# Kernel optimization log

Measured on AMD Instinct MI355X. Metric: run time of the kernel, lower is better.

The kernel has to match this reference:

```python
import jax, jax.numpy as jnp
import numpy as np
import math

# Equal-size graphs make SAGPooling's top-k static; removed edges are kept with a validity mask.
B, N0, D, H, HID, POS, DEG = 64, 400, 128, 4, 64, 16, 16
C = D // H                     # per-head dim = 32
EG = N0 * DEG                  # edges per graph
E = B * EG                     # 409600 edges total
RATIO = 0.8
K1 = math.ceil(RATIO * N0)     # 320
K2 = math.ceil(RATIO * K1)     # 256
K3 = math.ceil(RATIO * K2)     # 205
KS = (K1, K2, K3)
EPS = 1e-5

def _lin(x, W, b):
    return x @ W + b

def _ln(x, g, b):
    mu = x.mean(-1, keepdims=True)
    var = ((x - mu) ** 2).mean(-1, keepdims=True)
    return (x - mu) * jax.lax.rsqrt(var + EPS) * g + b

def _bn(x, g, b):  # BatchNorm1d, training mode (biased batch variance)
    mu = x.mean(0)
    var = ((x - mu) ** 2).mean(0)
    return (x - mu) * jax.lax.rsqrt(var + EPS) * g + b

def _transformer_conv(x, src, dst, mask, Wq, bq, Wk, bk, Wv, bv, Ws, bs, N):
    # PyG TransformerConv (concat=True, root_weight=True): scatter-softmax attention over edges
    q = _lin(x, Wq, bq).reshape(N, H, C)
    k = _lin(x, Wk, bk).reshape(N, H, C)
    v = _lin(x, Wv, bv).reshape(N, H, C)
    logits = jnp.einsum('ehc,ehc->eh', q[dst], k[src]) / jnp.sqrt(jnp.float32(C))
    logits = jnp.where(mask[:, None], logits, -1e9)
    m = jnp.maximum(jax.ops.segment_max(logits, dst, num_segments=N), -1e9)
    w = jnp.exp(logits - m[dst]) * mask[:, None]
    denom = jax.ops.segment_sum(w, dst, num_segments=N)
    alpha = w / jnp.where(denom[dst] > 0, denom[dst], 1.0)  # [E,H]
    msg = jax.ops.segment_sum(v[src] * alpha[:, :, None], dst, num_segments=N)
    return msg.reshape(N, D) + _lin(x, Ws, bs)

def _gt_block(x, src, dst, mask, Wq, bq, Wk, bk, Wv, bv, Ws, bs,
              Wlo, blo, g1, be1, W1, b1, W2, b2, g2, be2, N):
    out1 = _lin(_transformer_conv(x, src, dst, mask, Wq, bq, Wk, bk, Wv, bv, Ws, bs, N), Wlo, blo)
    out2 = _ln(out1 + x, g1, be1)
    out3 = _lin(jax.nn.relu(_lin(out2, W1, b1)), W2, b2)
    return _ln(out3 + out2, g2, be2)

def _sag_pool(x, src, dst, mask, Wrel, brel, Wroot, n, k):
    # SAGPooling: GraphConv(aggr='add') scorer, tanh nonlinearity, per-graph top-k, filter_adj via mask
    Nn = B * n
    agg = jax.ops.segment_sum(x[src] * mask[:, None], dst, num_segments=Nn)
    s = jnp.tanh((agg @ Wrel + brel + x @ Wroot)[:, 0])
    tv, ti = jax.lax.top_k(s.reshape(B, n), k)  # [B,k]
    perm = (ti + jnp.arange(B, dtype=ti.dtype)[:, None] * n).reshape(-1)
    x_new = x[perm] * tv.reshape(-1, 1)
    kept = jnp.zeros(Nn, bool).at[perm].set(True)
    new_id = jnp.zeros(Nn, jnp.int32).at[perm].set(jnp.arange(B * k, dtype=jnp.int32))
    nm = mask & kept[src] & kept[dst]
    return x_new, jnp.where(nm, new_id[src], 0), jnp.where(nm, new_id[dst], 0), nm

def _forward(x, lap_pos_enc, W_pos, b_pos,
             gt_Wq, gt_bq, gt_Wk, gt_bk, gt_Wv, gt_bv, gt_Wskip, gt_bskip,
             gt_Wlo, gt_blo, gt_ln1g, gt_ln1b, gt_W1, gt_b1, gt_W2, gt_b2, gt_ln2g, gt_ln2b,
             pool_Wrel, pool_brel, pool_Wroot,
             hW1, hb1, hW2, hb2, hW3, hb3, bn1g, bn1b, bn2g, bn2b,
             edge_src, edge_dst):
    x = x + _lin(lap_pos_enc, W_pos, b_pos)
    src, dst = edge_src, edge_dst
    mask = jnp.ones(src.shape, bool)
    n = N0
    feats = []
    for i in range(3):
        x = _gt_block(x, src, dst, mask,
                      gt_Wq[i], gt_bq[i], gt_Wk[i], gt_bk[i], gt_Wv[i], gt_bv[i],
                      gt_Wskip[i], gt_bskip[i], gt_Wlo[i], gt_blo[i],
                      gt_ln1g[i], gt_ln1b[i], gt_W1[i], gt_b1[i], gt_W2[i], gt_b2[i],
                      gt_ln2g[i], gt_ln2b[i], B * n)
        x, src, dst, mask = _sag_pool(x, src, dst, mask, pool_Wrel[i], pool_brel[i], pool_Wroot[i], n, KS[i])
        n = KS[i]
        xg = x.reshape(B, n, D)
        feats.append(jnp.concatenate([xg.max(1), xg.mean(1)], axis=1))  # [B, 2D] = gmp | gap
    xf = feats[0] + feats[1] + feats[2]
    h = jax.nn.relu(_bn(_lin(xf, hW1, hb1), bn1g, bn1b))
    h = jax.nn.relu(_bn(_lin(h, hW2, hb2), bn2g, bn2b))
    return _lin(h, hW3, hb3)[:, 0]  # [B]

def setup_inputs():
    key = jax.random.key(0)
    ks = jax.random.split(key, 16)
    rn = lambda k, shape, fan: jax.random.normal(k, shape, jnp.float32) / np.float32(np.sqrt(fan))
    inp = {}
    inp['x'] = jax.random.normal(ks[0], (B * N0, D), jnp.float32)
    inp['lap_pos_enc'] = jax.random.normal(ks[1], (B * N0, POS), jnp.float32)
    offs = (jnp.arange(B, dtype=jnp.int32) * N0)[:, None]
    inp['edge_src'] = (jax.random.randint(ks[2], (B, EG), 0, N0, jnp.int32) + offs).reshape(-1)
    inp['edge_dst'] = (jax.random.randint(ks[3], (B, EG), 0, N0, jnp.int32) + offs).reshape(-1)
    inp['W_pos'] = rn(ks[4], (POS, D), POS); inp['b_pos'] = jnp.zeros(D)
    pk = jax.random.split(ks[5], 12)
    inp['gt_Wq'] = rn(pk[0], (3, D, D), D); inp['gt_bq'] = jnp.zeros((3, D))
    inp['gt_Wk'] = rn(pk[1], (3, D, D), D); inp['gt_bk'] = jnp.zeros((3, D))
    inp['gt_Wv'] = rn(pk[2], (3, D, D), D); inp['gt_bv'] = jnp.zeros((3, D))
    inp['gt_Wskip'] = rn(pk[3], (3, D, D), D); inp['gt_bskip'] = jnp.zeros((3, D))
    inp['gt_Wlo'] = rn(pk[4], (3, D, D), D); inp['gt_blo'] = jnp.zeros((3, D))
    inp['gt_ln1g'] = jnp.ones((3, D)); inp['gt_ln1b'] = jnp.zeros((3, D))
    inp['gt_W1'] = rn(pk[5], (3, D, HID), D); inp['gt_b1'] = jnp.zeros((3, HID))
    inp['gt_W2'] = rn(pk[6], (3, HID, D), HID); inp['gt_b2'] = jnp.zeros((3, D))
    inp['gt_ln2g'] = jnp.ones((3, D)); inp['gt_ln2b'] = jnp.zeros((3, D))
    inp['pool_Wrel'] = rn(pk[7], (3, D, 1), D); inp['pool_brel'] = jnp.zeros((3, 1))
    inp['pool_Wroot'] = rn(pk[8], (3, D, 1), D)
    inp['hW1'] = rn(pk[9], (2 * D, D), 2 * D); inp['hb1'] = jnp.zeros(D)
    inp['hW2'] = rn(pk[10], (D, D // 2), D); inp['hb2'] = jnp.zeros(D // 2)
    inp['hW3'] = rn(pk[11], (D // 2, 1), D // 2); inp['hb3'] = jnp.zeros(1)
    inp['bn1g'] = jnp.ones(D); inp['bn1b'] = jnp.zeros(D)
    inp['bn2g'] = jnp.ones(D // 2); inp['bn2b'] = jnp.zeros(D // 2)
    return inp

def reference(x, lap_pos_enc, edge_src, edge_dst, W_pos, b_pos,
              gt_Wq, gt_bq, gt_Wk, gt_bk, gt_Wv, gt_bv, gt_Wskip, gt_bskip,
              gt_Wlo, gt_blo, gt_ln1g, gt_ln1b, gt_W1, gt_b1, gt_W2, gt_b2, gt_ln2g, gt_ln2b,
              pool_Wrel, pool_brel, pool_Wroot,
              hW1, hb1, hW2, hb2, hW3, hb3, bn1g, bn1b, bn2g, bn2b):
    return _forward(x, lap_pos_enc, W_pos, b_pos,
                    gt_Wq, gt_bq, gt_Wk, gt_bk, gt_Wv, gt_bv, gt_Wskip, gt_bskip,
                    gt_Wlo, gt_blo, gt_ln1g, gt_ln1b, gt_W1, gt_b1, gt_W2, gt_b2, gt_ln2g, gt_ln2b,
                    pool_Wrel, pool_brel, pool_Wroot,
                    hW1, hb1, hW2, hb2, hW3, hb3, bn1g, bn1b, bn2g, bn2b,
                    edge_src, edge_dst)
```

## Files before the change

### kernel.cpp

```cpp
#include <hip/hip_runtime.h>
#include <math.h>

#define BB   64
#define NPG0 400
#define DD   128
#define HH   4
#define CC   32
#define HIDD 64
#define POSD 16
#define EE   409600
#define EG   6400

__global__ void k_pos(const float* __restrict__ x, const float* __restrict__ lap,
                      const float* __restrict__ Wp, const float* __restrict__ bp,
                      float* __restrict__ out, int N){
  __shared__ float W[POSD*DD];
  __shared__ float bsh[DD];
  for(int i=threadIdx.x;i<POSD*DD;i+=blockDim.x) W[i]=Wp[i];
  for(int i=threadIdx.x;i<DD;i+=blockDim.x) bsh[i]=bp[i];
  __syncthreads();
  int total=N*DD;
  for(int idx=blockIdx.x*blockDim.x+threadIdx.x; idx<total; idx+=gridDim.x*blockDim.x){
    int n=idx>>7, d=idx&127;
    const float* lr=lap+(size_t)n*POSD;
    float acc=bsh[d]+x[idx];
    #pragma unroll
    for(int p=0;p<POSD;p++) acc=fmaf(lr[p],W[p*DD+d],acc);
    out[idx]=acc;
  }
}


template<int DIN,int DOUT,int EPI>
__global__ __launch_bounds__(512) void k_gemm_sw(
    const float* __restrict__ X, const float* __restrict__ Wg,
    const float* __restrict__ bias, const float* __restrict__ resid,
    const float* __restrict__ gam, const float* __restrict__ bet,
    float* __restrict__ Y){
  constexpr int CPW=DOUT/8;
  constexpr int NCG=CPW/4;
  constexpr int XPAD=DIN+4;
  __shared__ float Xl[64*XPAD];
  __shared__ float redA[8*64];
  __shared__ float redB[8*64];
  int tid=threadIdx.x;
  { const float4* xs=(const float4*)(X+(size_t)blockIdx.x*64*DIN);
    for(int i=tid;i<64*DIN/4;i+=512){
      int r=i/(DIN/4), kq=i%(DIN/4);
      *(float4*)&Xl[r*XPAD+kq*4]=xs[i];
    } }
  __syncthreads();
  int lane=tid&63;
  int wv=__builtin_amdgcn_readfirstlane(tid>>6);
  int cbase=wv*CPW;
  float acc[CPW];
  #pragma unroll
  for(int c=0;c<CPW;c++) acc[c]=0.f;
  const float* xr=&Xl[lane*XPAD];
  #pragma unroll 2
  for(int kt=0;kt<DIN/4;kt++){
    float4 xv=*(const float4*)&xr[4*kt];
    float xk[4]={xv.x,xv.y,xv.z,xv.w};
    #pragma unroll
    for(int kk=0;kk<4;kk++){
      const float4* wrow=(const float4*)(Wg+(size_t)(4*kt+kk)*DOUT+cbase);
      #pragma unroll
      for(int cg=0;cg<NCG;cg++){
        float4 w4=wrow[cg];
        acc[cg*4+0]=fmaf(xk[kk],w4.x,acc[cg*4+0]);
        acc[cg*4+1]=fmaf(xk[kk],w4.y,acc[cg*4+1]);
        acc[cg*4+2]=fmaf(xk[kk],w4.z,acc[cg*4+2]);
        acc[cg*4+3]=fmaf(xk[kk],w4.w,acc[cg*4+3]);
      }
    }
  }
  int row=blockIdx.x*64+lane;
  const float4* bb4=(const float4*)(bias+cbase);
  #pragma unroll
  for(int cg=0;cg<NCG;cg++){
    float4 b4=bb4[cg];
    acc[cg*4+0]+=b4.x; acc[cg*4+1]+=b4.y; acc[cg*4+2]+=b4.z; acc[cg*4+3]+=b4.w;
  }
  if(EPI==1){
    #pragma unroll
    for(int c=0;c<CPW;c++) acc[c]=fmaxf(acc[c],0.f);
  }
  if(EPI==2){
    #pragma unroll
    for(int cg=0;cg<NCG;cg++){
      float4 rv=*(const float4*)&resid[(size_t)row*DOUT+cbase+cg*4];
      acc[cg*4+0]+=rv.x; acc[cg*4+1]+=rv.y; acc[cg*4+2]+=rv.z; acc[cg*4+3]+=rv.w;
    }
    float ps=0.f,pq=0.f;
    #pragma unroll
    for(int c=0;c<CPW;c++){ ps+=acc[c]; pq+=acc[c]*acc[c]; }
    redA[wv*64+lane]=ps; redB[wv*64+lane]=pq;
    __syncthreads();
    float s=0.f,q=0.f;
    #pragma unroll
    for(int w=0;w<8;w++){ s+=redA[w*64+lane]; q+=redB[w*64+lane]; }
    float mu=s*(1.f/DOUT);
    float var=q*(1.f/DOUT)-mu*mu;
    float inv=1.0f/sqrtf(var+1e-5f);
    const float4* g4p=(const float4*)(gam+cbase);
    const float4* e4p=(const float4*)(bet+cbase);
    #pragma unroll
    for(int cg=0;cg<NCG;cg++){
      float4 g4=g4p[cg], e4=e4p[cg];
      acc[cg*4+0]=(acc[cg*4+0]-mu)*inv*g4.x+e4.x;
      acc[cg*4+1]=(acc[cg*4+1]-mu)*inv*g4.y+e4.y;
      acc[cg*4+2]=(acc[cg*4+2]-mu)*inv*g4.z+e4.z;
      acc[cg*4+3]=(acc[cg*4+3]-mu)*inv*g4.w+e4.w;
    }
  }
  #pragma unroll
  for(int cg=0;cg<NCG;cg++){
    float4 v; v.x=acc[cg*4+0]; v.y=acc[cg*4+1]; v.z=acc[cg*4+2]; v.w=acc[cg*4+3];
    *(float4*)&Y[(size_t)row*DOUT+cbase+cg*4]=v;
  }
}

__global__ __launch_bounds__(512) void k_gemm4_sw(
    const float* __restrict__ X,
    const float* __restrict__ W0,const float* __restrict__ W1,
    const float* __restrict__ W2,const float* __restrict__ W3,
    const float* __restrict__ b0,const float* __restrict__ b1,
    const float* __restrict__ b2,const float* __restrict__ b3,
    float* __restrict__ Y0,float* __restrict__ Y1,
    float* __restrict__ Y2,float* __restrict__ Y3){
  constexpr int XPAD=DD+4;
  __shared__ float Xl[64*XPAD];
  int tid=threadIdx.x;
  { const float4* xs=(const float4*)(X+(size_t)blockIdx.x*64*DD);
    for(int i=tid;i<64*32;i+=512){
      int r=i>>5, kq=i&31;
      *(float4*)&Xl[r*XPAD+kq*4]=xs[i];
    } }
  __syncthreads();
  int lane=tid&63;
  int wv=__builtin_amdgcn_readfirstlane(tid>>6);
  int cbase=wv*16;
  int row=blockIdx.x*64+lane;
  const float* xr=&Xl[lane*XPAD];
  auto one=[&](const float* __restrict__ Wg,const float* __restrict__ bias,float* __restrict__ Y){
    float acc[16];
    #pragma unroll
    for(int c=0;c<16;c++) acc[c]=0.f;
    #pragma unroll 2
    for(int kt=0;kt<32;kt++){
      float4 xv=*(const float4*)&xr[4*kt];
      float xk[4]={xv.x,xv.y,xv.z,xv.w};
      #pragma unroll
      for(int kk=0;kk<4;kk++){
        const float4* wrow=(const float4*)(Wg+(size_t)(4*kt+kk)*DD+cbase);
        #pragma unroll
        for(int cg=0;cg<4;cg++){
          float4 w4=wrow[cg];
          acc[cg*4+0]=fmaf(xk[kk],w4.x,acc[cg*4+0]);
          acc[cg*4+1]=fmaf(xk[kk],w4.y,acc[cg*4+1]);
          acc[cg*4+2]=fmaf(xk[kk],w4.z,acc[cg*4+2]);
          acc[cg*4+3]=fmaf(xk[kk],w4.w,acc[cg*4+3]);
        }
      }
    }
    const float4* bb4=(const float4*)(bias+cbase);
    #pragma unroll
    for(int cg=0;cg<4;cg++){
      float4 b4=bb4[cg];
      float4 v;
      v.x=acc[cg*4+0]+b4.x; v.y=acc[cg*4+1]+b4.y;
      v.z=acc[cg*4+2]+b4.z; v.w=acc[cg*4+3]+b4.w;
      *(float4*)&Y[(size_t)row*DD+cbase+cg*4]=v;
    }
  };
  one(W0,b0,Y0);
  one(W1,b1,Y1);
  one(W2,b2,Y2);
  one(W3,b3,Y3);
}

__global__ __launch_bounds__(512) void k_csr(const int* __restrict__ src,const int* __restrict__ dst,
   const int* __restrict__ msk,const int* __restrict__ kept,const int* __restrict__ nid,int n,
   int* __restrict__ rowstart,int* __restrict__ rowcnt,int* __restrict__ esrc,
   int* __restrict__ nsrc,int* __restrict__ ndst,int* __restrict__ nmsk){
  __shared__ int cnt[512];
  __shared__ int woff[512];
  int b=blockIdx.x, t=threadIdx.x;
  cnt[t]=0;
  __syncthreads();
  int ebase=b*EG, nbase=b*n;
  for(int j=t;j<EG;j+=512){
    int e=ebase+j;
    int s,d,m;
    if(kept){
      int s0=src[e], d0=dst[e];
      m=(msk?msk[e]:1) && kept[s0] && kept[d0];
      s=m?nid[s0]:0; d=m?nid[d0]:0;
      nsrc[e]=s; ndst[e]=d; nmsk[e]=m;
    } else { s=src[e]; d=dst[e]; m=1; }
    if(m) atomicAdd(&cnt[d-nbase],1);
  }
  __syncthreads();
  int v=cnt[t];
  woff[t]=v;
  __syncthreads();
  for(int off=1;off<512;off<<=1){
    int a=(t>=off)?woff[t-off]:0;
    __syncthreads();
    woff[t]+=a;
    __syncthreads();
  }
  int excl=woff[t]-v;
  if(t<n){ rowstart[nbase+t]=ebase+excl; rowcnt[nbase+t]=v; }
  __syncthreads();
  woff[t]=excl;
  __syncthreads();
  for(int j=t;j<EG;j+=512){
    int e=ebase+j;
    int s,d,m;
    if(kept){ m=nmsk[e]; s=nsrc[e]; d=ndst[e]; }
    else { m=1; s=src[e]; d=dst[e]; }
    if(!m) continue;
    int off=atomicAdd(&woff[d-nbase],1);
    esrc[ebase+off]=s;
  }
}

template<int NG>
__global__ __launch_bounds__(512) void k_attn4(const float* __restrict__ q,const float* __restrict__ kk,
     const float* __restrict__ v,const int* __restrict__ rowstart,const int* __restrict__ rowcnt,
     const int* __restrict__ esrc,float* __restrict__ attn){
  __shared__ float4 kl[NG*9];
  __shared__ float4 vl[NG*9];
  int b=blockIdx.x>>2, h=blockIdx.x&3;
  int nb=b*NG;
  const float4* kg=(const float4*)kk;
  const float4* vg=(const float4*)v;
  for(int i=threadIdx.x;i<NG*8;i+=512){
    int node=i>>3, qq=i&7;
    size_t gidx=(size_t)(nb+node)*32 + h*8 + qq;
    kl[node*9+qq]=kg[gidx];
    vl[node*9+qq]=vg[gidx];
  }
  __syncthreads();
  int node=threadIdx.x;
  if(node>=NG) return;
  int gn=nb+node;
  float4 q0,q1,q2,q3,q4,q5,q6,q7;
  { const float4* qp=(const float4*)(q+(size_t)gn*DD+h*CC);
    q0=qp[0];q1=qp[1];q2=qp[2];q3=qp[3];q4=qp[4];q5=qp[5];q6=qp[6];q7=qp[7]; }
  int st=rowstart[gn], cn=rowcnt[gn];
  float m=-1e30f, s=0.f;
  float4 o0={0,0,0,0},o1={0,0,0,0},o2={0,0,0,0},o3={0,0,0,0};
  float4 o4={0,0,0,0},o5={0,0,0,0},o6={0,0,0,0},o7={0,0,0,0};
  for(int j=0;j<cn;j++){
    int sl=esrc[st+j]-nb;
    const float4* kr=&kl[sl*9];
    float4 k0=kr[0],k1=kr[1],k2=kr[2],k3=kr[3],k4=kr[4],k5=kr[5],k6=kr[6],k7=kr[7];
    float a0=q0.x*k0.x+q0.y*k0.y+q0.z*k0.z+q0.w*k0.w;
    float a1=q1.x*k1.x+q1.y*k1.y+q1.z*k1.z+q1.w*k1.w;
    float a2=q2.x*k2.x+q2.y*k2.y+q2.z*k2.z+q2.w*k2.w;
    float a3=q3.x*k3.x+q3.y*k3.y+q3.z*k3.z+q3.w*k3.w;
    a0+=q4.x*k4.x+q4.y*k4.y+q4.z*k4.z+q4.w*k4.w;
    a1+=q5.x*k5.x+q5.y*k5.y+q5.z*k5.z+q5.w*k5.w;
    a2+=q6.x*k6.x+q6.y*k6.y+q6.z*k6.z+q6.w*k6.w;
    a3+=q7.x*k7.x+q7.y*k7.y+q7.z*k7.z+q7.w*k7.w;
    float lg=((a0+a1)+(a2+a3))*0.17677669529663687f;
    const float4* vr=&vl[sl*9];
    float4 v0=vr[0],v1=vr[1],v2=vr[2],v3=vr[3],v4=vr[4],v5=vr[5],v6=vr[6],v7=vr[7];
    if(lg<=m){
      float w=__expf(lg-m);
      s+=w;
      o0.x=fmaf(w,v0.x,o0.x);o0.y=fmaf(w,v0.y,o0.y);o0.z=fmaf(w,v0.z,o0.z);o0.w=fmaf(w,v0.w,o0.w);
      o1.x=fmaf(w,v1.x,o1.x);o1.y=fmaf(w,v1.y,o1.y);o1.z=fmaf(w,v1.z,o1.z);o1.w=fmaf(w,v1.w,o1.w);
      o2.x=fmaf(w,v2.x,o2.x);o2.y=fmaf(w,v2.y,o2.y);o2.z=fmaf(w,v2.z,o2.z);o2.w=fmaf(w,v2.w,o2.w);
      o3.x=fmaf(w,v3.x,o3.x);o3.y=fmaf(w,v3.y,o3.y);o3.z=fmaf(w,v3.z,o3.z);o3.w=fmaf(w,v3.w,o3.w);
      o4.x=fmaf(w,v4.x,o4.x);o4.y=fmaf(w,v4.y,o4.y);o4.z=fmaf(w,v4.z,o4.z);o4.w=fmaf(w,v4.w,o4.w);
      o5.x=fmaf(w,v5.x,o5.x);o5.y=fmaf(w,v5.y,o5.y);o5.z=fmaf(w,v5.z,o5.z);o5.w=fmaf(w,v5.w,o5.w);
      o6.x=fmaf(w,v6.x,o6.x);o6.y=fmaf(w,v6.y,o6.y);o6.z=fmaf(w,v6.z,o6.z);o6.w=fmaf(w,v6.w,o6.w);
      o7.x=fmaf(w,v7.x,o7.x);o7.y=fmaf(w,v7.y,o7.y);o7.z=fmaf(w,v7.z,o7.z);o7.w=fmaf(w,v7.w,o7.w);
    } else {
      float r=__expf(m-lg);
      s=fmaf(s,r,1.f);
      o0.x=fmaf(o0.x,r,v0.x);o0.y=fmaf(o0.y,r,v0.y);o0.z=fmaf(o0.z,r,v0.z);o0.w=fmaf(o0.w,r,v0.w);
      o1.x=fmaf(o1.x,r,v1.x);o1.y=fmaf(o1.y,r,v1.y);o1.z=fmaf(o1.z,r,v1.z);o1.w=fmaf(o1.w,r,v1.w);
      o2.x=fmaf(o2.x,r,v2.x);o2.y=fmaf(o2.y,r,v2.y);o2.z=fmaf(o2.z,r,v2.z);o2.w=fmaf(o2.w,r,v2.w);
      o3.x=fmaf(o3.x,r,v3.x);o3.y=fmaf(o3.y,r,v3.y);o3.z=fmaf(o3.z,r,v3.z);o3.w=fmaf(o3.w,r,v3.w);
      o4.x=fmaf(o4.x,r,v4.x);o4.y=fmaf(o4.y,r,v4.y);o4.z=fmaf(o4.z,r,v4.z);o4.w=fmaf(o4.w,r,v4.w);
      o5.x=fmaf(o5.x,r,v5.x);o5.y=fmaf(o5.y,r,v5.y);o5.z=fmaf(o5.z,r,v5.z);o5.w=fmaf(o5.w,r,v5.w);
      o6.x=fmaf(o6.x,r,v6.x);o6.y=fmaf(o6.y,r,v6.y);o6.z=fmaf(o6.z,r,v6.z);o6.w=fmaf(o6.w,r,v6.w);
      o7.x=fmaf(o7.x,r,v7.x);o7.y=fmaf(o7.y,r,v7.y);o7.z=fmaf(o7.z,r,v7.z);o7.w=fmaf(o7.w,r,v7.w);
      m=lg;
    }
  }
  float inv=(s>0.f)?(1.f/s):0.f;
  float* op=attn+(size_t)gn*DD+h*CC;
  float4* op4=(float4*)op;
  float4 r0=op4[0],r1=op4[1],r2=op4[2],r3=op4[3],r4=op4[4],r5=op4[5],r6=op4[6],r7=op4[7];
  r0.x+=o0.x*inv;r0.y+=o0.y*inv;r0.z+=o0.z*inv;r0.w+=o0.w*inv;
  r1.x+=o1.x*inv;r1.y+=o1.y*inv;r1.z+=o1.z*inv;r1.w+=o1.w*inv;
  r2.x+=o2.x*inv;r2.y+=o2.y*inv;r2.z+=o2.z*inv;r2.w+=o2.w*inv;
  r3.x+=o3.x*inv;r3.y+=o3.y*inv;r3.z+=o3.z*inv;r3.w+=o3.w*inv;
  r4.x+=o4.x*inv;r4.y+=o4.y*inv;r4.z+=o4.z*inv;r4.w+=o4.w*inv;
  r5.x+=o5.x*inv;r5.y+=o5.y*inv;r5.z+=o5.z*inv;r5.w+=o5.w*inv;
  r6.x+=o6.x*inv;r6.y+=o6.y*inv;r6.z+=o6.z*inv;r6.w+=o6.w*inv;
  r7.x+=o7.x*inv;r7.y+=o7.y*inv;r7.z+=o7.z*inv;r7.w+=o7.w*inv;
  op4[0]=r0;op4[1]=r1;op4[2]=r2;op4[3]=r3;op4[4]=r4;op4[5]=r5;op4[6]=r6;op4[7]=r7;
}

__global__ __launch_bounds__(512) void k_sagtopk(const float* __restrict__ x,
   const float* __restrict__ wrel,const float* __restrict__ wroot,const float* __restrict__ brel,
   const int* __restrict__ rowstart,const int* __restrict__ rowcnt,const int* __restrict__ esrc,
   int n,int k,float* __restrict__ tv,int* __restrict__ gi,
   int* __restrict__ kept,int* __restrict__ nid){
  __shared__ float pnl[NPG0];
  __shared__ float sv[512];
  __shared__ int   si[512];
  int b=blockIdx.x, t=threadIdx.x, nbase=b*n;
  float rdot=0.f;
  if(t<n){
    const float4* xr=(const float4*)(x+(size_t)(nbase+t)*DD);
    float p=0.f;
    #pragma unroll
    for(int qq=0;qq<32;qq++){
      float4 xv=xr[qq];
      float4 wr=((const float4*)wrel)[qq];
      float4 wo=((const float4*)wroot)[qq];
      p   =fmaf(xv.x,wr.x,fmaf(xv.y,wr.y,fmaf(xv.z,wr.z,fmaf(xv.w,wr.w,p))));
      rdot=fmaf(xv.x,wo.x,fmaf(xv.y,wo.y,fmaf(xv.z,wo.z,fmaf(xv.w,wo.w,rdot))));
    }
    pnl[t]=p;
  }
  __syncthreads();
  float sc=-INFINITY;
  if(t<n){
    int st=rowstart[nbase+t], cn=rowcnt[nbase+t];
    float s=0.f;
    for(int j=0;j<cn;j++) s+=pnl[esrc[st+j]-nbase];
    sc=tanhf(s+brel[0]+rdot);
  }
  sv[t]=(t<n)?sc:-INFINITY;
  si[t]=t;
  for(int ksz=2;ksz<=512;ksz<<=1){
    for(int j=ksz>>1;j>0;j>>=1){
      __syncthreads();
      int ixj=t^j;
      if(ixj>t){
        float s1=sv[t], s2=sv[ixj];
        int i1=si[t], i2=si[ixj];
        bool firstRanks=(s1>s2)||(s1==s2&&i1<i2);
        bool up=((t&ksz)==0);
        if(up? !firstRanks : firstRanks){ sv[t]=s2;sv[ixj]=s1;si[t]=i2;si[ixj]=i1; }
      }
    }
  }
  __syncthreads();
  if(t<k){
    int oldg=nbase+si[t];
    tv[b*k+t]=sv[t];
    gi[b*k+t]=oldg;
    kept[oldg]=1;
    nid[oldg]=b*k+t;
  } else if(t<n){
    kept[nbase+si[t]]=0;
  }
}

__global__ void k_gather(const float* __restrict__ xin, const int* __restrict__ gi,
                         const float* __restrict__ tv, float* __restrict__ xout, int rows){
  int idx=blockIdx.x*blockDim.x+threadIdx.x;
  if(idx>=rows*DD) return;
  int r=idx>>7;
  int d=idx&127;
  xout[idx]=xin[(size_t)gi[r]*DD+d]*tv[r];
}

__global__ __launch_bounds__(512) void k_readout(const float* __restrict__ xk, int k,
                                                 float* __restrict__ xf){
  __shared__ float pm[512];
  __shared__ float ps[512];
  int b=blockIdx.x, t=threadIdx.x;
  int d=t&127, strip=t>>7;
  const float* base=xk+((size_t)b*k)*DD+d;
  float mx=-INFINITY, sm=0.f;
  for(int j=strip;j<k;j+=4){
    float v=base[(size_t)j*DD];
    mx=fmaxf(mx,v); sm+=v;
  }
  pm[t]=mx; ps[t]=sm;
  __syncthreads();
  if(t<128){
    float m0=fmaxf(fmaxf(pm[t],pm[t+128]),fmaxf(pm[t+256],pm[t+384]));
    float s0=ps[t]+ps[t+128]+ps[t+256]+ps[t+384];
    xf[b*256+t]+=m0;
    xf[b*256+128+t]+=s0/(float)k;
  }
}

__global__ void k_h1(const float* __restrict__ xf,const float* __restrict__ W,const float* __restrict__ b,float* __restrict__ z){
  int i=blockIdx.x*blockDim.x+threadIdx.x; if(i>=BB*DD) return;
  int r=i>>7, j=i&127;
  float acc=b[j];
  const float* xr=xf+r*256;
  #pragma unroll 8
  for(int t=0;t<256;t++) acc=fmaf(xr[t], W[t*DD+j], acc);
  z[i]=acc;
}
__global__ void k_bnrelu(const float* __restrict__ z,const float* __restrict__ g,const float* __restrict__ be,
                         float* __restrict__ h,int cols){
  int j=blockIdx.x*blockDim.x+threadIdx.x; if(j>=cols) return;
  float mu=0.f;
  for(int r=0;r<BB;r++) mu+=z[r*cols+j];
  mu*=(1.f/BB);
  float var=0.f;
  for(int r=0;r<BB;r++){ float d=z[r*cols+j]-mu; var+=d*d; }
  var*=(1.f/BB);
  float inv=1.0f/sqrtf(var+1e-5f);
  float gg=g[j], bb=be[j];
  for(int r=0;r<BB;r++){ float y=(z[r*cols+j]-mu)*inv*gg+bb; h[r*cols+j]=fmaxf(y,0.f); }
}
__global__ void k_h2(const float* __restrict__ h1,const float* __restrict__ W,const float* __restrict__ b,float* __restrict__ z){
  int i=blockIdx.x*blockDim.x+threadIdx.x; if(i>=BB*HIDD) return;
  int r=i>>6, j=i&63;
  float acc=b[j];
  #pragma unroll 8
  for(int t=0;t<DD;t++) acc=fmaf(h1[r*DD+t], W[t*HIDD+j], acc);
  z[i]=acc;
}
__global__ void k_h3(const float* __restrict__ h2,const float* __restrict__ W,const float* __restrict__ b,float* __restrict__ out){
  int bi=threadIdx.x; if(bi>=BB) return;
  float acc=b[0];
  for(int t=0;t<HIDD;t++) acc=fmaf(h2[bi*HIDD+t], W[t], acc);
  out[bi]=acc;
}

extern "C" void kernel_launch(void* const* d_in, const int* in_sizes, int n_in,
                              void* d_out, int out_size, void* d_ws, size_t ws_size,
                              hipStream_t stream){
  (void)in_sizes; (void)n_in; (void)out_size; (void)ws_size;
  const float* x_in =(const float*)d_in[0];
  const float* lap  =(const float*)d_in[1];
  const int*   esrc0=(const int*)  d_in[2];
  const int*   edst0=(const int*)  d_in[3];
  const float* Wpos =(const float*)d_in[4];
  const float* bpos =(const float*)d_in[5];
  const float* gWq  =(const float*)d_in[6];
  const float* gbq  =(const float*)d_in[7];
  const float* gWk  =(const float*)d_in[8];
  const float* gbk  =(const float*)d_in[9];
  const float* gWv  =(const float*)d_in[10];
  const float* gbv  =(const float*)d_in[11];
  const float* gWs  =(const float*)d_in[12];
  const float* gbs  =(const float*)d_in[13];
  const float* gWlo =(const float*)d_in[14];
  const float* gblo =(const float*)d_in[15];
  const float* gl1g =(const float*)d_in[16];
  const float* gl1b =(const float*)d_in[17];
  const float* gW1  =(const float*)d_in[18];
  const float* gb1  =(const float*)d_in[19];
  const float* gW2  =(const float*)d_in[20];
  const float* gb2  =(const float*)d_in[21];
  const float* gl2g =(const float*)d_in[22];
  const float* gl2b =(const float*)d_in[23];
  const float* pWrel=(const float*)d_in[24];
  const float* pbrel=(const float*)d_in[25];
  const float* pWrt =(const float*)d_in[26];
  const float* hW1  =(const float*)d_in[27];
  const float* hb1  =(const float*)d_in[28];
  const float* hW2  =(const float*)d_in[29];
  const float* hb2  =(const float*)d_in[30];
  const float* hW3  =(const float*)d_in[31];
  const float* hb3  =(const float*)d_in[32];
  const float* bn1g =(const float*)d_in[33];
  const float* bn1b =(const float*)d_in[34];
  const float* bn2g =(const float*)d_in[35];
  const float* bn2b =(const float*)d_in[36];
  float* out=(float*)d_out;

  char* base=(char*)d_ws; size_t off=0;
  auto alloc=[&](size_t bytes)->void*{ void* p=base+off; off+=(bytes+255)&~(size_t)255; return p; };
  const int NMAX=BB*NPG0;
  float* xA  =(float*)alloc((size_t)NMAX*DD*4);
  float* qb  =(float*)alloc((size_t)NMAX*DD*4);
  float* kb  =(float*)alloc((size_t)NMAX*DD*4);
  float* vb  =(float*)alloc((size_t)NMAX*DD*4);
  float* xO  =(float*)alloc((size_t)NMAX*DD*4);
  float* t2  =(float*)alloc((size_t)NMAX*DD*4);
  int*   rowstart=(int*)alloc((size_t)NMAX*4);
  int*   rowcnt  =(int*)alloc((size_t)NMAX*4);
  int*   esrcW   =(int*)alloc((size_t)EE*4);
  float* tvb =(float*)alloc((size_t)BB*320*4);
  int*   gib =(int*)  alloc((size_t)BB*320*4);
  int*   kept=(int*)  alloc((size_t)NMAX*4);
  int*   nid =(int*)  alloc((size_t)NMAX*4);
  int*   srcA=(int*)  alloc((size_t)EE*4);
  int*   dstA=(int*)  alloc((size_t)EE*4);
  int*   mskA=(int*)  alloc((size_t)EE*4);
  int*   srcB=(int*)  alloc((size_t)EE*4);
  int*   dstB=(int*)  alloc((size_t)EE*4);
  int*   mskB=(int*)  alloc((size_t)EE*4);
  float* xf  =(float*)alloc((size_t)BB*256*4);
  float* z1  =(float*)alloc((size_t)BB*DD*4);
  float* h1b =(float*)alloc((size_t)BB*DD*4);
  float* z2  =(float*)alloc((size_t)BB*HIDD*4);
  float* h2b =(float*)alloc((size_t)BB*HIDD*4);

  const int npg[3]={400,320,256};
  const int kpg[3]={320,256,205};
  const int Nin[3]={BB*400, BB*320, BB*256};

  hipMemsetAsync(xf,0,(size_t)BB*256*4,stream);
  k_pos<<<2048,256,0,stream>>>(x_in,lap,Wpos,bpos,xA,Nin[0]);

  const int* src=esrc0; const int* dst=edst0; const int* msk=nullptr;

  for(int i=0;i<3;i++){
    int N=Nin[i];
    int gB=N/64;
    const float* Wq=gWq+(size_t)i*DD*DD;   const float* bq=gbq+(size_t)i*DD;
    const float* Wk=gWk+(size_t)i*DD*DD;   const float* bk=gbk+(size_t)i*DD;
    const float* Wv=gWv+(size_t)i*DD*DD;   const float* bv=gbv+(size_t)i*DD;
    const float* Ws=gWs+(size_t)i*DD*DD;   const float* bs=gbs+(size_t)i*DD;
    const float* Wlo=gWlo+(size_t)i*DD*DD; const float* blo=gblo+(size_t)i*DD;
    const float* l1g=gl1g+(size_t)i*DD;    const float* l1b=gl1b+(size_t)i*DD;
    const float* W1=gW1+(size_t)i*DD*HIDD; const float* b1=gb1+(size_t)i*HIDD;
    const float* W2=gW2+(size_t)i*HIDD*DD; const float* b2=gb2+(size_t)i*DD;
    const float* l2g=gl2g+(size_t)i*DD;    const float* l2b=gl2b+(size_t)i*DD;
    const float* wrel=pWrel+(size_t)i*DD;  const float* brel=pbrel+(size_t)i;
    const float* wrt=pWrt+(size_t)i*DD;

    if(i==0){
      k_csr<<<BB,512,0,stream>>>(src,dst,nullptr,nullptr,nullptr,npg[i],
                                 rowstart,rowcnt,esrcW,nullptr,nullptr,nullptr);
    } else {
      int* ns=(i==1)?srcA:srcB; int* ndd=(i==1)?dstA:dstB; int* nm=(i==1)?mskA:mskB;
      k_csr<<<BB,512,0,stream>>>(src,dst,msk,kept,nid,npg[i],
                                 rowstart,rowcnt,esrcW,ns,ndd,nm);
      src=ns; dst=ndd; msk=nm;
    }

    k_gemm4_sw<<<gB,512,0,stream>>>(xA,Wq,Wk,Wv,Ws,bq,bk,bv,bs,qb,kb,vb,xO);
    if(i==0)      k_attn4<400><<<BB*HH,512,0,stream>>>(qb,kb,vb,rowstart,rowcnt,esrcW,xO);
    else if(i==1) k_attn4<320><<<BB*HH,512,0,stream>>>(qb,kb,vb,rowstart,rowcnt,esrcW,xO);
    else          k_attn4<256><<<BB*HH,512,0,stream>>>(qb,kb,vb,rowstart,rowcnt,esrcW,xO);
    k_gemm_sw<128,128,2><<<gB,512,0,stream>>>(xO,Wlo,blo,xA,l1g,l1b,t2);
    k_gemm_sw<128,64,1><<<gB,512,0,stream>>>(t2,W1,b1,nullptr,nullptr,nullptr,qb);
    k_gemm_sw<64,128,2><<<gB,512,0,stream>>>(qb,W2,b2,t2,l2g,l2b,xO);

    k_sagtopk<<<BB,512,0,stream>>>(xO,wrel,wrt,brel,rowstart,rowcnt,esrcW,
                                   npg[i],kpg[i],tvb,gib,kept,nid);
    int rows=BB*kpg[i];
    k_gather<<<(rows*DD+255)/256,256,0,stream>>>(xO,gib,tvb,xA,rows);
    k_readout<<<BB,512,0,stream>>>(xA,kpg[i],xf);
  }

  k_h1<<<(BB*DD+127)/128,128,0,stream>>>(xf,hW1,hb1,z1);
  k_bnrelu<<<1,128,0,stream>>>(z1,bn1g,bn1b,h1b,DD);
  k_h2<<<(BB*HIDD+127)/128,128,0,stream>>>(h1b,hW2,hb2,z2);
  k_bnrelu<<<1,64,0,stream>>>(z2,bn2g,bn2b,h2b,HIDD);
  k_h3<<<1,64,0,stream>>>(h2b,hW3,hb3,out);
}
```

Before: 595.4 us.

## Fuse output projection, LayerNorms and FFN into one kernel per block

Replaces the three separate GEMM launches (output projection with residual+LN, FFN up-projection with ReLU, FFN down-projection with residual+LN) with a single kernel. It keeps the per-row intermediates (LN1 output and hidden activations) in shared memory. This removes two launches and the global round-trips of the t2 and hidden buffers. The QKV GEMM's inner loop is also restructured to preload eight float4 chunks of X from LDS before the FMAs. The fused kernel writes in place to xO, which is safe because each block reads only its own rows into LDS before any write. It uses more shared memory per block, which may lower occupancy.

```diff
diff --git a/kernel.cpp b/kernel.cpp
--- a/kernel.cpp
+++ b/kernel.cpp
@@ -30,95 +30,6 @@
   }
 }
 
-
-template<int DIN,int DOUT,int EPI>
-__global__ __launch_bounds__(512) void k_gemm_sw(
-    const float* __restrict__ X, const float* __restrict__ Wg,
-    const float* __restrict__ bias, const float* __restrict__ resid,
-    const float* __restrict__ gam, const float* __restrict__ bet,
-    float* __restrict__ Y){
-  constexpr int CPW=DOUT/8;
-  constexpr int NCG=CPW/4;
-  constexpr int XPAD=DIN+4;
-  __shared__ float Xl[64*XPAD];
-  __shared__ float redA[8*64];
-  __shared__ float redB[8*64];
-  int tid=threadIdx.x;
-  { const float4* xs=(const float4*)(X+(size_t)blockIdx.x*64*DIN);
-    for(int i=tid;i<64*DIN/4;i+=512){
-      int r=i/(DIN/4), kq=i%(DIN/4);
-      *(float4*)&Xl[r*XPAD+kq*4]=xs[i];
-    } }
-  __syncthreads();
-  int lane=tid&63;
-  int wv=__builtin_amdgcn_readfirstlane(tid>>6);
-  int cbase=wv*CPW;
-  float acc[CPW];
-  #pragma unroll
-  for(int c=0;c<CPW;c++) acc[c]=0.f;
-  const float* xr=&Xl[lane*XPAD];
-  #pragma unroll 2
-  for(int kt=0;kt<DIN/4;kt++){
-    float4 xv=*(const float4*)&xr[4*kt];
-    float xk[4]={xv.x,xv.y,xv.z,xv.w};
-    #pragma unroll
-    for(int kk=0;kk<4;kk++){
-      const float4* wrow=(const float4*)(Wg+(size_t)(4*kt+kk)*DOUT+cbase);
-      #pragma unroll
-      for(int cg=0;cg<NCG;cg++){
-        float4 w4=wrow[cg];
-        acc[cg*4+0]=fmaf(xk[kk],w4.x,acc[cg*4+0]);
-        acc[cg*4+1]=fmaf(xk[kk],w4.y,acc[cg*4+1]);
-        acc[cg*4+2]=fmaf(xk[kk],w4.z,acc[cg*4+2]);
-        acc[cg*4+3]=fmaf(xk[kk],w4.w,acc[cg*4+3]);
-      }
-    }
-  }
-  int row=blockIdx.x*64+lane;
-  const float4* bb4=(const float4*)(bias+cbase);
-  #pragma unroll
-  for(int cg=0;cg<NCG;cg++){
-    float4 b4=bb4[cg];
-    acc[cg*4+0]+=b4.x; acc[cg*4+1]+=b4.y; acc[cg*4+2]+=b4.z; acc[cg*4+3]+=b4.w;
-  }
-  if(EPI==1){
-    #pragma unroll
-    for(int c=0;c<CPW;c++) acc[c]=fmaxf(acc[c],0.f);
-  }
-  if(EPI==2){
-    #pragma unroll
-    for(int cg=0;cg<NCG;cg++){
-      float4 rv=*(const float4*)&resid[(size_t)row*DOUT+cbase+cg*4];
-      acc[cg*4+0]+=rv.x; acc[cg*4+1]+=rv.y; acc[cg*4+2]+=rv.z; acc[cg*4+3]+=rv.w;
-    }
-    float ps=0.f,pq=0.f;
-    #pragma unroll
-    for(int c=0;c<CPW;c++){ ps+=acc[c]; pq+=acc[c]*acc[c]; }
-    redA[wv*64+lane]=ps; redB[wv*64+lane]=pq;
-    __syncthreads();
-    float s=0.f,q=0.f;
-    #pragma unroll
-    for(int w=0;w<8;w++){ s+=redA[w*64+lane]; q+=redB[w*64+lane]; }
-    float mu=s*(1.f/DOUT);
-    float var=q*(1.f/DOUT)-mu*mu;
-    float inv=1.0f/sqrtf(var+1e-5f);
-    const float4* g4p=(const float4*)(gam+cbase);
-    const float4* e4p=(const float4*)(bet+cbase);
-    #pragma unroll
-    for(int cg=0;cg<NCG;cg++){
-      float4 g4=g4p[cg], e4=e4p[cg];
-      acc[cg*4+0]=(acc[cg*4+0]-mu)*inv*g4.x+e4.x;
-      acc[cg*4+1]=(acc[cg*4+1]-mu)*inv*g4.y+e4.y;
-      acc[cg*4+2]=(acc[cg*4+2]-mu)*inv*g4.z+e4.z;
-      acc[cg*4+3]=(acc[cg*4+3]-mu)*inv*g4.w+e4.w;
-    }
-  }
-  #pragma unroll
-  for(int cg=0;cg<NCG;cg++){
-    float4 v; v.x=acc[cg*4+0]; v.y=acc[cg*4+1]; v.z=acc[cg*4+2]; v.w=acc[cg*4+3];
-    *(float4*)&Y[(size_t)row*DOUT+cbase+cg*4]=v;
-  }
-}
 
 __global__ __launch_bounds__(512) void k_gemm4_sw(
     const float* __restrict__ X,
@@ -147,12 +58,84 @@
     #pragma unroll
     for(int c=0;c<16;c++) acc[c]=0.f;
     #pragma unroll 2
-    for(int kt=0;kt<32;kt++){
-      float4 xv=*(const float4*)&xr[4*kt];
-      float xk[4]={xv.x,xv.y,xv.z,xv.w};
+    for(int ch=0;ch<4;ch++){
+      float4 xq[8];
+      #pragma unroll
+      for(int q=0;q<8;q++) xq[q]=*(const float4*)&xr[ch*32+4*q];
+      #pragma unroll
+      for(int q=0;q<8;q++){
+        float xk[4]={xq[q].x,xq[q].y,xq[q].z,xq[q].w};
+        #pragma unroll
+        for(int kk=0;kk<4;kk++){
+          const float4* wrow=(const float4*)(Wg+(size_t)(ch*32+q*4+kk)*DD+cbase);
+          #pragma unroll
+          for(int cg=0;cg<4;cg++){
+            float4 w4=wrow[cg];
+            acc[cg*4+0]=fmaf(xk[kk],w4.x,acc[cg*4+0]);
+            acc[cg*4+1]=fmaf(xk[kk],w4.y,acc[cg*4+1]);
+            acc[cg*4+2]=fmaf(xk[kk],w4.z,acc[cg*4+2]);
+            acc[cg*4+3]=fmaf(xk[kk],w4.w,acc[cg*4+3]);
+          }
+        }
+      }
+    }
+    const float4* bb4=(const float4*)(bias+cbase);
+    #pragma unroll
+    for(int cg=0;cg<4;cg++){
+      float4 b4=bb4[cg];
+      float4 v;
+      v.x=acc[cg*4+0]+b4.x; v.y=acc[cg*4+1]+b4.y;
+      v.z=acc[cg*4+2]+b4.z; v.w=acc[cg*4+3]+b4.w;
+      *(float4*)&Y[(size_t)row*DD+cbase+cg*4]=v;
+    }
+  };
+  one(W0,b0,Y0);
+  one(W1,b1,Y1);
+  one(W2,b2,Y2);
+  one(W3,b3,Y3);
+}
+
+__global__ __launch_bounds__(512) void k_ffn_fused(
+    const float* __restrict__ Xg, const float* __restrict__ resid,
+    const float* __restrict__ Wlo, const float* __restrict__ blo,
+    const float* __restrict__ l1g, const float* __restrict__ l1b,
+    const float* __restrict__ W1, const float* __restrict__ b1,
+    const float* __restrict__ W2, const float* __restrict__ b2,
+    const float* __restrict__ l2g, const float* __restrict__ l2b,
+    float* __restrict__ Y){
+  constexpr int XPAD=DD+4;
+  constexpr int HPAD=HIDD+4;
+  __shared__ float Xa[64*XPAD];
+  __shared__ float hb[64*HPAD];
+  __shared__ float redA[8*64];
+  __shared__ float redB[8*64];
+  int tid=threadIdx.x;
+  { const float4* xs=(const float4*)(Xg+(size_t)blockIdx.x*64*DD);
+    for(int i=tid;i<64*32;i+=512){
+      int r=i>>5, kq=i&31;
+      *(float4*)&Xa[r*XPAD+kq*4]=xs[i];
+    } }
+  __syncthreads();
+  int lane=tid&63;
+  int wv=__builtin_amdgcn_readfirstlane(tid>>6);
+  int row=blockIdx.x*64+lane;
+  const float* xr=&Xa[lane*XPAD];
+
+  int cbase=wv*16;
+  float acc[16];
+  #pragma unroll
+  for(int c=0;c<16;c++) acc[c]=0.f;
+  #pragma unroll 2
+  for(int ch=0;ch<4;ch++){
+    float4 xq[8];
+    #pragma unroll
+    for(int q=0;q<8;q++) xq[q]=*(const float4*)&xr[ch*32+4*q];
+    #pragma unroll
+    for(int q=0;q<8;q++){
+      float xk[4]={xq[q].x,xq[q].y,xq[q].z,xq[q].w};
       #pragma unroll
       for(int kk=0;kk<4;kk++){
-        const float4* wrow=(const float4*)(Wg+(size_t)(4*kt+kk)*DD+cbase);
+        const float4* wrow=(const float4*)(Wlo+(size_t)(ch*32+q*4+kk)*DD+cbase);
         #pragma unroll
         for(int cg=0;cg<4;cg++){
           float4 w4=wrow[cg];
@@ -163,20 +146,133 @@
         }
       }
     }
-    const float4* bb4=(const float4*)(bias+cbase);
+  }
+  { const float4* bb4=(const float4*)(blo+cbase);
     #pragma unroll
     for(int cg=0;cg<4;cg++){
       float4 b4=bb4[cg];
+      float4 rv=*(const float4*)&resid[(size_t)row*DD+cbase+cg*4];
+      acc[cg*4+0]+=b4.x+rv.x; acc[cg*4+1]+=b4.y+rv.y;
+      acc[cg*4+2]+=b4.z+rv.z; acc[cg*4+3]+=b4.w+rv.w;
+    } }
+  { float ps=0.f,pq=0.f;
+    #pragma unroll
+    for(int c=0;c<16;c++){ ps+=acc[c]; pq+=acc[c]*acc[c]; }
+    redA[wv*64+lane]=ps; redB[wv*64+lane]=pq;
+    __syncthreads();
+    float s=0.f,q=0.f;
+    #pragma unroll
+    for(int w=0;w<8;w++){ s+=redA[w*64+lane]; q+=redB[w*64+lane]; }
+    float mu=s*(1.f/DD);
+    float inv=1.0f/sqrtf(q*(1.f/DD)-mu*mu+1e-5f);
+    const float4* g4p=(const float4*)(l1g+cbase);
+    const float4* e4p=(const float4*)(l1b+cbase);
+    #pragma unroll
+    for(int cg=0;cg<4;cg++){
+      float4 g4=g4p[cg], e4=e4p[cg];
       float4 v;
-      v.x=acc[cg*4+0]+b4.x; v.y=acc[cg*4+1]+b4.y;
-      v.z=acc[cg*4+2]+b4.z; v.w=acc[cg*4+3]+b4.w;
+      v.x=(acc[cg*4+0]-mu)*inv*g4.x+e4.x;
+      v.y=(acc[cg*4+1]-mu)*inv*g4.y+e4.y;
+      v.z=(acc[cg*4+2]-mu)*inv*g4.z+e4.z;
+      v.w=(acc[cg*4+3]-mu)*inv*g4.w+e4.w;
+      *(float4*)&Xa[lane*XPAD+cbase+cg*4]=v;
+    } }
+  __syncthreads();
+
+  { int cb2=wv*8;
+    float acc2[8];
+    #pragma unroll
+    for(int c=0;c<8;c++) acc2[c]=0.f;
+    #pragma unroll 2
+    for(int ch=0;ch<4;ch++){
+      float4 xq[8];
+      #pragma unroll
+      for(int q=0;q<8;q++) xq[q]=*(const float4*)&xr[ch*32+4*q];
+      #pragma unroll
+      for(int q=0;q<8;q++){
+        float xk[4]={xq[q].x,xq[q].y,xq[q].z,xq[q].w};
+        #pragma unroll
+        for(int kk=0;kk<4;kk++){
+          const float4* wrow=(const float4*)(W1+(size_t)(ch*32+q*4+kk)*HIDD+cb2);
+          #pragma unroll
+          for(int cg=0;cg<2;cg++){
+            float4 w4=wrow[cg];
+            acc2[cg*4+0]=fmaf(xk[kk],w4.x,acc2[cg*4+0]);
+            acc2[cg*4+1]=fmaf(xk[kk],w4.y,acc2[cg*4+1]);
+            acc2[cg*4+2]=fmaf(xk[kk],w4.z,acc2[cg*4+2]);
+            acc2[cg*4+3]=fmaf(xk[kk],w4.w,acc2[cg*4+3]);
+          }
+        }
+      }
+    }
+    const float4* bb4=(const float4*)(b1+cb2);
+    #pragma unroll
+    for(int cg=0;cg<2;cg++){
+      float4 b4=bb4[cg];
+      float4 v;
+      v.x=fmaxf(acc2[cg*4+0]+b4.x,0.f); v.y=fmaxf(acc2[cg*4+1]+b4.y,0.f);
+      v.z=fmaxf(acc2[cg*4+2]+b4.z,0.f); v.w=fmaxf(acc2[cg*4+3]+b4.w,0.f);
+      *(float4*)&hb[lane*HPAD+cb2+cg*4]=v;
+    } }
+  __syncthreads();
+
+  { float acc3[16];
+    #pragma unroll
+    for(int c=0;c<16;c++) acc3[c]=0.f;
+    const float* hr=&hb[lane*HPAD];
+    #pragma unroll 2
+    for(int ch=0;ch<2;ch++){
+      float4 xq[8];
+      #pragma unroll
+      for(int q=0;q<8;q++) xq[q]=*(const float4*)&hr[ch*32+4*q];
+      #pragma unroll
+      for(int q=0;q<8;q++){
+        float xk[4]={xq[q].x,xq[q].y,xq[q].z,xq[q].w};
+        #pragma unroll
+        for(int kk=0;kk<4;kk++){
+          const float4* wrow=(const float4*)(W2+(size_t)(ch*32+q*4+kk)*DD+cbase);
+          #pragma unroll
+          for(int cg=0;cg<4;cg++){
+            float4 w4=wrow[cg];
+            acc3[cg*4+0]=fmaf(xk[kk],w4.x,acc3[cg*4+0]);
+            acc3[cg*4+1]=fmaf(xk[kk],w4.y,acc3[cg*4+1]);
+            acc3[cg*4+2]=fmaf(xk[kk],w4.z,acc3[cg*4+2]);
+            acc3[cg*4+3]=fmaf(xk[kk],w4.w,acc3[cg*4+3]);
+          }
+        }
+      }
+    }
+    const float4* bb4=(const float4*)(b2+cbase);
+    #pragma unroll
+    for(int cg=0;cg<4;cg++){
+      float4 b4=bb4[cg];
+      float4 rv=*(const float4*)&Xa[lane*XPAD+cbase+cg*4];
+      acc3[cg*4+0]+=b4.x+rv.x; acc3[cg*4+1]+=b4.y+rv.y;
+      acc3[cg*4+2]+=b4.z+rv.z; acc3[cg*4+3]+=b4.w+rv.w;
+    }
+    float ps=0.f,pq=0.f;
+    #pragma unroll
+    for(int c=0;c<16;c++){ ps+=acc3[c]; pq+=acc3[c]*acc3[c]; }
+    __syncthreads();
+    redA[wv*64+lane]=ps; redB[wv*64+lane]=pq;
+    __syncthreads();
+    float s=0.f,q=0.f;
+    #pragma unroll
+    for(int w=0;w<8;w++){ s+=redA[w*64+lane]; q+=redB[w*64+lane]; }
+    float mu=s*(1.f/DD);
+    float inv=1.0f/sqrtf(q*(1.f/DD)-mu*mu+1e-5f);
+    const float4* g4p=(const float4*)(l2g+cbase);
+    const float4* e4p=(const float4*)(l2b+cbase);
+    #pragma unroll
+    for(int cg=0;cg<4;cg++){
+      float4 g4=g4p[cg], e4=e4p[cg];
+      float4 v;
+      v.x=(acc3[cg*4+0]-mu)*inv*g4.x+e4.x;
+      v.y=(acc3[cg*4+1]-mu)*inv*g4.y+e4.y;
+      v.z=(acc3[cg*4+2]-mu)*inv*g4.z+e4.z;
+      v.w=(acc3[cg*4+3]-mu)*inv*g4.w+e4.w;
       *(float4*)&Y[(size_t)row*DD+cbase+cg*4]=v;
-    }
-  };
-  one(W0,b0,Y0);
-  one(W1,b1,Y1);
-  one(W2,b2,Y2);
-  one(W3,b3,Y3);
+    } }
 }
 
 __global__ __launch_bounds__(512) void k_csr(const int* __restrict__ src,const int* __restrict__ dst,
@@ -485,7 +581,6 @@
   float* kb  =(float*)alloc((size_t)NMAX*DD*4);
   float* vb  =(float*)alloc((size_t)NMAX*DD*4);
   float* xO  =(float*)alloc((size_t)NMAX*DD*4);
-  float* t2  =(float*)alloc((size_t)NMAX*DD*4);
   int*   rowstart=(int*)alloc((size_t)NMAX*4);
   int*   rowcnt  =(int*)alloc((size_t)NMAX*4);
   int*   esrcW   =(int*)alloc((size_t)EE*4);
@@ -543,9 +638,7 @@
     if(i==0)      k_attn4<400><<<BB*HH,512,0,stream>>>(qb,kb,vb,rowstart,rowcnt,esrcW,xO);
     else if(i==1) k_attn4<320><<<BB*HH,512,0,stream>>>(qb,kb,vb,rowstart,rowcnt,esrcW,xO);
     else          k_attn4<256><<<BB*HH,512,0,stream>>>(qb,kb,vb,rowstart,rowcnt,esrcW,xO);
-    k_gemm_sw<128,128,2><<<gB,512,0,stream>>>(xO,Wlo,blo,xA,l1g,l1b,t2);
-    k_gemm_sw<128,64,1><<<gB,512,0,stream>>>(t2,W1,b1,nullptr,nullptr,nullptr,qb);
-    k_gemm_sw<64,128,2><<<gB,512,0,stream>>>(qb,W2,b2,t2,l2g,l2b,xO);
+    k_ffn_fused<<<gB,512,0,stream>>>(xO,xA,Wlo,blo,l1g,l1b,W1,b1,W2,b2,l2g,l2b,xO);
 
     k_sagtopk<<<BB,512,0,stream>>>(xO,wrel,wrt,brel,rowstart,rowcnt,esrcW,
                                    npg[i],kpg[i],tvb,gib,kept,nid);
```

Result: no change. 594.6 us (-0.1%).
